# Kernel optimization log

Measured on AMD Instinct MI355X. Metric: run time of the kernel, lower is better.

The kernel has to match this reference:

```python
import jax, jax.numpy as jnp
import numpy as np

HIDDEN = 768
NUM_BLOCKS = 8
BLOCK = HIDDEN // NUM_BLOCKS
BASE_THR, K_DECAY, MIN_THR = 0.01, 20.0, 0.0005


def _threshold(height, width):
    # wavenumber-dependent soft-shrink threshold T(k), shape [H, W//2+1]
    fu = jnp.fft.fftfreq(height, d=1.0).astype(jnp.float32)[:, None]
    fv = jnp.fft.rfftfreq(width, d=1.0).astype(jnp.float32)[None, :]
    k = jnp.sqrt(fu ** 2 + fv ** 2) * max(height, width)
    thr = BASE_THR * jnp.exp(-0.5 * (k / K_DECAY) ** 2)
    return jnp.maximum(thr, MIN_THR)


def setup_inputs() -> dict:
    key = jax.random.key(0)
    kx, k1, k2, k3, k4 = jax.random.split(key, 5)
    scale = 0.02
    x = jax.random.normal(kx, (4, 128, 128, HIDDEN), dtype=jnp.float32)
    w1 = scale * jax.random.normal(k1, (2, NUM_BLOCKS, BLOCK, BLOCK), dtype=jnp.float32)
    b1 = scale * jax.random.normal(k2, (2, NUM_BLOCKS, BLOCK), dtype=jnp.float32)
    w2 = scale * jax.random.normal(k3, (2, NUM_BLOCKS, BLOCK, BLOCK), dtype=jnp.float32)
    b2 = scale * jax.random.normal(k4, (2, NUM_BLOCKS, BLOCK), dtype=jnp.float32)
    return {"x": x, "w1": w1, "b1": b1, "w2": w2, "b2": b2}


def reference(x, w1, b1, w2, b2):
    dtype = x.dtype
    bias = x
    xf = x.astype(jnp.float32)
    B, H, W, C = xf.shape
    Wc = W // 2 + 1
    # rfft2 over spatial dims, orthonormal
    Xc = jnp.fft.rfft2(xf, axes=(1, 2), norm='ortho')
    Xc = Xc.reshape(B, H, Wc, NUM_BLOCKS, BLOCK)
    xr, xi = jnp.real(Xc), jnp.imag(Xc)
    mm = lambda t, w: jnp.einsum('bhwni,nio->bhwno', t, w)
    # complex block-diagonal 2-layer MLP
    o1r = jax.nn.relu(mm(xr, w1[0]) - mm(xi, w1[1]) + b1[0])
    o1i = jax.nn.relu(mm(xi, w1[0]) + mm(xr, w1[1]) + b1[1])
    o2r = mm(o1r, w2[0]) - mm(o1i, w2[1]) + b2[0]
    o2i = mm(o1i, w2[0]) + mm(o1r, w2[1]) + b2[1]
    # soft-shrink on complex magnitude with wavenumber-dependent threshold
    mag = jnp.sqrt(o2r ** 2 + o2i ** 2 + 1e-8)
    thr = _threshold(H, W)[None, :, :, None, None]  # [1,H,Wc,1,1]
    sf = jax.nn.relu(mag - thr) / mag
    Yc = (o2r * sf) + 1j * (o2i * sf)
    Yc = Yc.reshape(B, H, Wc, C)
    y = jnp.fft.irfft2(Yc, s=(H, W), axes=(1, 2), norm='ortho')
    return y.astype(dtype) + bias
```

## Files before the change

kernel.cpp:

```cpp
#include <hip/hip_runtime.h>
#include <hip/hip_bf16.h>
#include <math.h>


#define HD   768
#define NBLK 8
#define HH   128
#define WW   128
#define WC   65
#define NPOS (HH * WC)

constexpr float SC    = 0.08838834764831845f;
constexpr float TWOPI = 6.28318530717958647692f;

constexpr int TM_OFF     = 0;
constexpr int TW_OFF     = 49152;
constexpr int TWI_OFF    = 69632;
constexpr int WF_OFF     = 90112;
constexpr int WF_END_U16 = 679936;
constexpr size_t A_UINTS = (size_t)4 * NPOS * HD;

typedef __attribute__((ext_vector_type(8))) short short8;
typedef __attribute__((ext_vector_type(4))) float f32x4;

#define MFMA __builtin_amdgcn_mfma_f32_16x16x32_bf16

static __device__ inline unsigned short f2bf(float f) {
  __hip_bfloat16 h = __float2bfloat16(f);
  return __builtin_bit_cast(unsigned short, h);
}
static __device__ inline unsigned int pack2(float re, float im) {
  return (unsigned int)f2bf(re) | ((unsigned int)f2bf(im) << 16);
}
static __device__ inline float lo2f(unsigned int u) {
  return __builtin_bit_cast(float, u << 16);
}
static __device__ inline float hi2f(unsigned int u) {
  return __builtin_bit_cast(float, u & 0xffff0000u);
}

__global__ __launch_bounds__(256) void k_prep(const float* __restrict__ w1,
                                              const float* __restrict__ b1,
                                              const float* __restrict__ w2,
                                              const float* __restrict__ b2,
                                              unsigned short* __restrict__ wf,
                                              float* __restrict__ bpk) {
  const int blk = blockIdx.x, t = threadIdx.x;
  if (blk < 16) {
    const int layer = blk >> 3, n = blk & 7;
    const float* w  = layer ? w2 : w1;
    const float* bs = layer ? b2 : b1;
    unsigned short* dst = wf + WF_OFF + (size_t)blk * (72 * 512);
    for (int e = t; e < 72 * 512; e += 256) {
      int f = e >> 9, idx = e & 511;
      int kk = f / 12, nt = f - kk * 12;
      int lane = idx >> 3, j = idx & 7;
      int k  = kk * 32 + (lane >> 4) * 8 + j;
      int cc = nt * 16 + (lane & 15);
      float v;
      if (k < 96) v = (cc < 96) ? w[(size_t)n * 9216 + k * 96 + cc]
                                : w[(size_t)(8 + n) * 9216 + k * 96 + (cc - 96)];
      else        v = (cc < 96) ? -w[(size_t)(8 + n) * 9216 + (k - 96) * 96 + cc]
                                :  w[(size_t)n * 9216 + (k - 96) * 96 + (cc - 96)];
      dst[e] = f2bf(v);
    }
    for (int c = t; c < 192; c += 256)
      bpk[blk * 192 + c] = (c < 96) ? bs[n * 96 + c] : bs[(8 + n) * 96 + (c - 96)];
  } else if (blk == 16) {
    for (int e = t; e < 96 * 512; e += 256) {
      int f = e >> 9, idx = e & 511;
      int part = f >> 5, rem = f & 31, kot = rem >> 2, kk = rem & 3;
      int lane = idx >> 3, j = idx & 7;
      int ko = kot * 16 + (lane & 15);
      int r  = kk * 32 + (lane >> 4) * 8 + j;
      float sn, cs; sincosf((TWOPI / 128.f) * (float)((ko * r) & 127), &sn, &cs);
      float v = (part == 0) ? cs : (part == 1) ? sn : -sn;
      wf[TM_OFF + (size_t)f * 512 + idx] = f2bf(v * SC);
    }
  } else if (blk == 17) {
    for (int e = t; e < 40 * 512; e += 256) {
      int f = e >> 9, idx = e & 511;
      int mt = f >> 2, kk = f & 3;
      int lane = idx >> 3, j = idx & 7;
      int row = mt * 16 + (lane & 15);
      int r   = kk * 32 + (lane >> 4) * 8 + j;
      int kor = (row < 80) ? row : row - 80;
      float sn, cs; sincosf((TWOPI / 128.f) * (float)((kor * r) & 127), &sn, &cs);
      wf[TW_OFF + (size_t)f * 512 + idx] = f2bf((row < 80 ? cs : -sn) * SC);
    }
  } else {
    for (int e = t; e < 40 * 512; e += 256) {
      int f = e >> 9, idx = e & 511;
      int mt = f / 5, kk = f - mt * 5;
      int lane = idx >> 3, j = idx & 7;
      int wr = mt * 16 + (lane & 15);
      int k  = kk * 32 + (lane >> 4) * 8 + j;
      float v = 0.f;
      if (k < 80) {
        int kb = k;
        if (kb <= 64) {
          float sn, cs; sincosf((TWOPI / 128.f) * (float)((wr * kb) & 127), &sn, &cs);
          v = SC * ((kb == 0 || kb == 64) ? 1.f : 2.f) * cs;
        }
      } else {
        int kb = k - 80;
        if (kb >= 1 && kb <= 63) {
          float sn, cs; sincosf((TWOPI / 128.f) * (float)((wr * kb) & 127), &sn, &cs);
          v = -2.f * SC * sn;
        }
      }
      wf[TWI_OFF + (size_t)f * 512 + idx] = f2bf(v);
    }
  }
}

__global__ __launch_bounds__(256) void k_fft_w(const float* __restrict__ x,
                                               unsigned int* __restrict__ A,
                                               const unsigned short* __restrict__ wf) {
  __shared__ unsigned short Xt[64 * 136];
  const int h = blockIdx.x, c0 = blockIdx.y * 64, b = blockIdx.z, t = threadIdx.x;
  const int wv = t >> 6, lane = t & 63, l15 = lane & 15, lg = lane >> 4;
  const float* xp = x + ((size_t)(b * HH + h)) * WW * HD + c0;
  for (int idx = t; idx < 128 * 64; idx += 256) {
    int r = idx >> 6, ch = idx & 63;
    Xt[ch * 136 + r] = f2bf(xp[(size_t)r * HD + ch]);
  }
  __syncthreads();
  const unsigned short* tw = wf + TW_OFF;
  f32x4 acc[10];
#pragma unroll
  for (int m = 0; m < 10; ++m) acc[m] = { 0.f, 0.f, 0.f, 0.f };
#pragma unroll
  for (int kk = 0; kk < 4; ++kk) {
    short8 bq = *(const short8*)&Xt[(wv * 16 + l15) * 136 + kk * 32 + lg * 8];
#pragma unroll
    for (int m = 0; m < 10; ++m) {
      short8 a = *(const short8*)&tw[(size_t)(m * 4 + kk) * 512 + lane * 8];
      acc[m] = MFMA(a, bq, acc[m], 0, 0, 0);
    }
  }
  unsigned int* Ao = A + ((size_t)b * NPOS + h * WC) * HD + c0 + wv * 16 + l15;
#pragma unroll
  for (int q = 0; q < 5; ++q)
#pragma unroll
    for (int r = 0; r < 4; ++r) {
      int ko = q * 16 + lg * 4 + r;
      if (ko <= 64) Ao[(size_t)ko * HD] = pack2(acc[q][r], acc[5 + q][r]);
    }
}

__global__ __launch_bounds__(256) void k_ifft_w(const unsigned int* __restrict__ A,
                                                const unsigned int* __restrict__ Bp,
                                                float* __restrict__ out,
                                                const unsigned short* __restrict__ wf) {
  __shared__ unsigned short Zt[64 * 168];
  const int h = blockIdx.x, c0 = blockIdx.y * 64, b = blockIdx.z, t = threadIdx.x;
  const int wv = t >> 6, lane = t & 63, l15 = lane & 15, lg = lane >> 4;
  const size_t base = ((size_t)b * NPOS + h * WC) * HD + c0;
  for (int idx = t; idx < 65 * 64; idx += 256) {
    int kb = idx >> 6, ch = idx & 63;
    unsigned int uA = A[base + (size_t)kb * HD + ch];
    unsigned int uB = Bp[base + (size_t)kb * HD + ch];
    float re = lo2f(uA) + lo2f(uB);
    float im = hi2f(uA) + hi2f(uB);
    Zt[ch * 168 + kb]      = f2bf(re);
    Zt[ch * 168 + 80 + kb] = (kb == 0 || kb == 64) ? (unsigned short)0 : f2bf(im);
  }
  for (int idx = t; idx < 64 * 32; idx += 256) {
    int ch = idx >> 5, q = idx & 31;
    if (q < 30) {
      int kb = 65 + (q % 15), half = q / 15;
      Zt[ch * 168 + half * 80 + kb] = 0;
    }
  }
  __syncthreads();
  const unsigned short* twi = wf + TWI_OFF;
  f32x4 acc[8];
#pragma unroll
  for (int m = 0; m < 8; ++m) acc[m] = { 0.f, 0.f, 0.f, 0.f };
#pragma unroll
  for (int kk = 0; kk < 5; ++kk) {
    short8 bq = *(const short8*)&Zt[(wv * 16 + l15) * 168 + kk * 32 + lg * 8];
#pragma unroll
    for (int m = 0; m < 8; ++m) {
      short8 a = *(const short8*)&twi[(size_t)(m * 5 + kk) * 512 + lane * 8];
      acc[m] = MFMA(a, bq, acc[m], 0, 0, 0);
    }
  }
#pragma unroll
  for (int m = 0; m < 8; ++m)
#pragma unroll
    for (int r = 0; r < 4; ++r) {
      int wr = m * 16 + lg * 4 + r;
      size_t go = (((size_t)(b * HH + h)) * WW + wr) * HD + c0 + wv * 16 + l15;
      out[go] = acc[m][r];
    }
}

template <int FWD>
static __device__ inline void dft_gemm8(const unsigned short* Rb, const unsigned short* Ib,
                                        const unsigned short* tm, int w, int lane,
                                        f32x4* aR, f32x4* aI) {
  const int l15 = lane & 15, lg = lane >> 4;
#pragma unroll
  for (int kkr = 0; kkr < 4; ++kkr) {
    const int r0 = kkr * 32 + lg * 8;
    short8 Ac = *(const short8*)&tm[(size_t)(0 * 32 + w * 4 + kkr) * 512 + lane * 8];
    short8 As = *(const short8*)&tm[(size_t)(1 * 32 + w * 4 + kkr) * 512 + lane * 8];
    short8 An = *(const short8*)&tm[(size_t)(2 * 32 + w * 4 + kkr) * 512 + lane * 8];
#pragma unroll
    for (int c = 0; c < 6; ++c) {
      short8 zr = *(const short8*)&Rb[(c * 16 + l15) * 136 + r0];
      short8 zi = *(const short8*)&Ib[(c * 16 + l15) * 136 + r0];
      aR[c] = MFMA(Ac, zr, aR[c], 0, 0, 0);
      if constexpr (FWD) {
        aR[c] = MFMA(As, zi, aR[c], 0, 0, 0);
        aI[c] = MFMA(Ac, zi, aI[c], 0, 0, 0);
        aI[c] = MFMA(An, zr, aI[c], 0, 0, 0);
      } else {
        aR[c] = MFMA(An, zi, aR[c], 0, 0, 0);
        aI[c] = MFMA(Ac, zi, aI[c], 0, 0, 0);
        aI[c] = MFMA(As, zr, aI[c], 0, 0, 0);
      }
    }
  }
}

__global__ __launch_bounds__(512) void k_mid(const unsigned int* __restrict__ A,
                                             unsigned int* __restrict__ Bp,
                                             const unsigned short* __restrict__ wf,
                                             const float* __restrict__ bpk) {
  __shared__ unsigned short Rb[13312], Ib[13312];
  __shared__ unsigned short WfX[2][12 * 512];
  const int kv = blockIdx.x, n = blockIdx.y, b = blockIdx.z, t = threadIdx.x;
  const int w = t >> 6, lane = t & 63, l15 = lane & 15, lg = lane >> 4;
  const size_t pbase = ((size_t)b * NPOS + kv) * HD + n * 96;
  const unsigned short* tm = wf + TM_OFF;
  const unsigned short* wf1 = wf + WF_OFF + (size_t)n * (72 * 512);
  const unsigned short* wf2 = wf + WF_OFF + (size_t)(8 + n) * (72 * 512);

#define LOAD_X(BUFI, SRC, KP)                                                    \
  for (int idx = t; idx < 768; idx += 512)                                       \
    ((int4*)WfX[BUFI])[idx] = ((const int4*)((SRC) + (KP) * 12 * 512))[idx];

  for (int idx = t; idx < 128 * 96; idx += 512) {
    int r = idx / 96, ch = idx - r * 96;
    unsigned int u = A[pbase + (size_t)r * (WC * HD) + ch];
    Rb[ch * 136 + r] = (unsigned short)(u & 0xffffu);
    Ib[ch * 136 + r] = (unsigned short)(u >> 16);
  }
  LOAD_X(0, wf1, 0);
  __syncthreads();

  f32x4 aR[6], aI[6];
#pragma unroll
  for (int c = 0; c < 6; ++c) { aR[c] = {0.f,0.f,0.f,0.f}; aI[c] = {0.f,0.f,0.f,0.f}; }
  dft_gemm8<1>(Rb, Ib, tm, w, lane, aR, aI);
  LOAD_X(1, wf1, 1);
  __syncthreads();

#pragma unroll
  for (int c = 0; c < 6; ++c)
#pragma unroll
    for (int r = 0; r < 4; ++r) {
      int row = w * 16 + lg * 4 + r, ch = c * 16 + l15;
      Rb[row * 104 + ch] = f2bf(aR[c][r]);
      Ib[row * 104 + ch] = f2bf(aI[c][r]);
    }

  const int row_a = (w * 16 + l15) * 104;
  f32x4 acc[12];
#pragma unroll
  for (int nt = 0; nt < 12; ++nt) {
    float bv = bpk[n * 192 + nt * 16 + l15];
    acc[nt] = { bv, bv, bv, bv };
  }

#define MLP_PAIR(BUF)                                                            \
  {                                                                              \
    short8 aRf = *(const short8*)&Rb[row_a + PK * 32 + lg * 8];                  \
    short8 aIf = *(const short8*)&Ib[row_a + PK * 32 + lg * 8];                  \
    _Pragma("unroll")                                                            \
    for (int nt = 0; nt < 12; ++nt) {                                            \
      short8 b0 = *(const short8*)&(BUF)[nt * 512 + lane * 8];                   \
      acc[nt] = MFMA(aRf, b0, acc[nt], 0, 0, 0);                                 \
      int nt2 = (nt < 6) ? nt + 6 : nt - 6;                                      \
      int4 nb = *(const int4*)&(BUF)[nt2 * 512 + lane * 8];                      \
      if (nt < 6) { nb.x ^= 0x80008000; nb.y ^= 0x80008000;                      \
                    nb.z ^= 0x80008000; nb.w ^= 0x80008000; }                    \
      acc[nt] = MFMA(aIf, __builtin_bit_cast(short8, nb), acc[nt], 0, 0, 0);     \
    }                                                                            \
  }

  { const int PK = 0; MLP_PAIR(WfX[0]); }
  { const int PK = 1; MLP_PAIR(WfX[1]); }
  __syncthreads();
  LOAD_X(0, wf1, 2);
  LOAD_X(1, wf2, 0);
  __syncthreads();
  { const int PK = 2; MLP_PAIR(WfX[0]); }

#pragma unroll
  for (int i = 0; i < 6; ++i)
#pragma unroll
    for (int r = 0; r < 4; ++r) {
      int row = w * 16 + lg * 4 + r, ch = i * 16 + l15;
      Rb[row * 104 + ch] = f2bf(fmaxf(acc[i][r], 0.f));
      Ib[row * 104 + ch] = f2bf(fmaxf(acc[6 + i][r], 0.f));
    }
#pragma unroll
  for (int nt = 0; nt < 12; ++nt) {
    float bv = bpk[(8 + n) * 192 + nt * 16 + l15];
    acc[nt] = { bv, bv, bv, bv };
  }
  __syncthreads();
  LOAD_X(0, wf2, 1);

  { const int PK = 0; MLP_PAIR(WfX[1]); }
  __syncthreads();
  LOAD_X(1, wf2, 2);
  { const int PK = 1; MLP_PAIR(WfX[0]); }
  __syncthreads();
  { const int PK = 2; MLP_PAIR(WfX[1]); }
  __syncthreads();

#pragma unroll
  for (int r = 0; r < 4; ++r) {
    int ko = w * 16 + lg * 4 + r;
    float kus = (ko >= 64) ? (float)(ko - 128) : (float)ko;
    float k2v = kus * kus + (float)(kv * kv);
    float thr = fmaxf(0.01f * expf(-0.00125f * k2v), 0.0005f);
#pragma unroll
    for (int i = 0; i < 6; ++i) {
      float mr = acc[i][r], mi = acc[6 + i][r];
      float mag = sqrtf(mr * mr + mi * mi + 1e-8f);
      float sf = fmaxf(mag - thr, 0.f) / mag;
      int ch = i * 16 + l15;
      Rb[ch * 136 + ko] = f2bf(mr * sf);
      Ib[ch * 136 + ko] = f2bf(mi * sf);
    }
  }
  __syncthreads();

#pragma unroll
  for (int c = 0; c < 6; ++c) { aR[c] = {0.f,0.f,0.f,0.f}; aI[c] = {0.f,0.f,0.f,0.f}; }
  dft_gemm8<0>(Rb, Ib, tm, w, lane, aR, aI);
#pragma unroll
  for (int c = 0; c < 6; ++c)
#pragma unroll
    for (int r = 0; r < 4; ++r) {
      int rr = w * 16 + lg * 4 + r, ch = c * 16 + l15;
      Bp[pbase + (size_t)rr * (WC * HD) + ch] = pack2(aR[c][r], aI[c][r]);
    }
#undef MLP_PAIR
#undef LOAD_X
}

extern "C" void kernel_launch(void* const* d_in, const int* in_sizes, int n_in,
                              void* d_out, int out_size, void* d_ws, size_t ws_size,
                              hipStream_t stream) {
  const float* x  = (const float*)d_in[0];
  const float* w1 = (const float*)d_in[1];
  const float* b1 = (const float*)d_in[2];
  const float* w2 = (const float*)d_in[3];
  const float* b2 = (const float*)d_in[4];
  float* out = (float*)d_out;
  unsigned int* A  = (unsigned int*)d_ws;
  unsigned int* Bp = A + A_UINTS;

  unsigned short* wf = (unsigned short*)(Bp + A_UINTS);
  float* bpk = (float*)(wf + WF_END_U16);

  k_prep<<<19, 256, 0, stream>>>(w1, b1, w2, b2, wf, bpk);
  k_fft_w<<<dim3(HH, HD / 64, 4), 256, 0, stream>>>(x, A, wf);
  k_mid<<<dim3(WC, NBLK, 4), 512, 0, stream>>>(A, Bp, wf, bpk);
  k_ifft_w<<<dim3(HH, HD / 64, 4), 256, 0, stream>>>(A, Bp, out, wf);
}
```

Measured before the change: 410.9 us.

## Single-buffer MLP weight tiles in LDS and XOR-swizzle spectral tiles

Replaces the double-buffered weight staging area with one buffer and adds barriers around each weight-chunk load, cutting LDS use per block by 12 KB, likely to fit more blocks per CU. It also applies an XOR swizzle to the channel-major spectral tiles used by the DFT GEMM to reduce LDS bank conflicts. The trade-off is that weight loads no longer overlap with MFMA work and the kernel has more syncthreads.

```diff
diff --git a/kernel.cpp b/kernel.cpp
--- a/kernel.cpp
+++ b/kernel.cpp
@@ -24,6 +24,8 @@
 typedef __attribute__((ext_vector_type(4))) float f32x4;
 
 #define MFMA __builtin_amdgcn_mfma_f32_16x16x32_bf16
+
+#define SWZ(ch, r) ((ch) * 136 + ((r) ^ (((ch) & 7) << 4)))
 
 static __device__ inline unsigned short f2bf(float f) {
   __hip_bfloat16 h = __float2bfloat16(f);
@@ -210,8 +212,9 @@
     short8 An = *(const short8*)&tm[(size_t)(2 * 32 + w * 4 + kkr) * 512 + lane * 8];
 #pragma unroll
     for (int c = 0; c < 6; ++c) {
-      short8 zr = *(const short8*)&Rb[(c * 16 + l15) * 136 + r0];
-      short8 zi = *(const short8*)&Ib[(c * 16 + l15) * 136 + r0];
+      const int ch = c * 16 + l15;
+      short8 zr = *(const short8*)&Rb[SWZ(ch, r0)];
+      short8 zi = *(const short8*)&Ib[SWZ(ch, r0)];
       aR[c] = MFMA(Ac, zr, aR[c], 0, 0, 0);
       if constexpr (FWD) {
         aR[c] = MFMA(As, zi, aR[c], 0, 0, 0);
@@ -231,7 +234,7 @@
                                              const unsigned short* __restrict__ wf,
                                              const float* __restrict__ bpk) {
   __shared__ unsigned short Rb[13312], Ib[13312];
-  __shared__ unsigned short WfX[2][12 * 512];
+  __shared__ unsigned short WfL[12 * 512];
   const int kv = blockIdx.x, n = blockIdx.y, b = blockIdx.z, t = threadIdx.x;
   const int w = t >> 6, lane = t & 63, l15 = lane & 15, lg = lane >> 4;
   const size_t pbase = ((size_t)b * NPOS + kv) * HD + n * 96;
@@ -239,24 +242,23 @@
   const unsigned short* wf1 = wf + WF_OFF + (size_t)n * (72 * 512);
   const unsigned short* wf2 = wf + WF_OFF + (size_t)(8 + n) * (72 * 512);
 
-#define LOAD_X(BUFI, SRC, KP)                                                    \
+#define LOAD_W(SRC, KP)                                                          \
   for (int idx = t; idx < 768; idx += 512)                                       \
-    ((int4*)WfX[BUFI])[idx] = ((const int4*)((SRC) + (KP) * 12 * 512))[idx];
+    ((int4*)WfL)[idx] = ((const int4*)((SRC) + (KP) * 12 * 512))[idx];
 
   for (int idx = t; idx < 128 * 96; idx += 512) {
     int r = idx / 96, ch = idx - r * 96;
     unsigned int u = A[pbase + (size_t)r * (WC * HD) + ch];
-    Rb[ch * 136 + r] = (unsigned short)(u & 0xffffu);
-    Ib[ch * 136 + r] = (unsigned short)(u >> 16);
-  }
-  LOAD_X(0, wf1, 0);
+    Rb[SWZ(ch, r)] = (unsigned short)(u & 0xffffu);
+    Ib[SWZ(ch, r)] = (unsigned short)(u >> 16);
+  }
+  LOAD_W(wf1, 0);
   __syncthreads();
 
   f32x4 aR[6], aI[6];
 #pragma unroll
   for (int c = 0; c < 6; ++c) { aR[c] = {0.f,0.f,0.f,0.f}; aI[c] = {0.f,0.f,0.f,0.f}; }
   dft_gemm8<1>(Rb, Ib, tm, w, lane, aR, aI);
-  LOAD_X(1, wf1, 1);
   __syncthreads();
 
 #pragma unroll
@@ -276,29 +278,31 @@
     acc[nt] = { bv, bv, bv, bv };
   }
 
-#define MLP_PAIR(BUF)                                                            \
+#define MLP_PAIR()                                                               \
   {                                                                              \
     short8 aRf = *(const short8*)&Rb[row_a + PK * 32 + lg * 8];                  \
     short8 aIf = *(const short8*)&Ib[row_a + PK * 32 + lg * 8];                  \
     _Pragma("unroll")                                                            \
     for (int nt = 0; nt < 12; ++nt) {                                            \
-      short8 b0 = *(const short8*)&(BUF)[nt * 512 + lane * 8];                   \
+      short8 b0 = *(const short8*)&WfL[nt * 512 + lane * 8];                     \
       acc[nt] = MFMA(aRf, b0, acc[nt], 0, 0, 0);                                 \
       int nt2 = (nt < 6) ? nt + 6 : nt - 6;                                      \
-      int4 nb = *(const int4*)&(BUF)[nt2 * 512 + lane * 8];                      \
+      int4 nb = *(const int4*)&WfL[nt2 * 512 + lane * 8];                        \
       if (nt < 6) { nb.x ^= 0x80008000; nb.y ^= 0x80008000;                      \
                     nb.z ^= 0x80008000; nb.w ^= 0x80008000; }                    \
       acc[nt] = MFMA(aIf, __builtin_bit_cast(short8, nb), acc[nt], 0, 0, 0);     \
     }                                                                            \
   }
 
-  { const int PK = 0; MLP_PAIR(WfX[0]); }
-  { const int PK = 1; MLP_PAIR(WfX[1]); }
-  __syncthreads();
-  LOAD_X(0, wf1, 2);
-  LOAD_X(1, wf2, 0);
-  __syncthreads();
-  { const int PK = 2; MLP_PAIR(WfX[0]); }
+  { const int PK = 0; MLP_PAIR(); }
+  __syncthreads();
+  LOAD_W(wf1, 1);
+  __syncthreads();
+  { const int PK = 1; MLP_PAIR(); }
+  __syncthreads();
+  LOAD_W(wf1, 2);
+  __syncthreads();
+  { const int PK = 2; MLP_PAIR(); }
 
 #pragma unroll
   for (int i = 0; i < 6; ++i)
@@ -314,14 +318,18 @@
     acc[nt] = { bv, bv, bv, bv };
   }
   __syncthreads();
-  LOAD_X(0, wf2, 1);
-
-  { const int PK = 0; MLP_PAIR(WfX[1]); }
-  __syncthreads();
-  LOAD_X(1, wf2, 2);
-  { const int PK = 1; MLP_PAIR(WfX[0]); }
-  __syncthreads();
-  { const int PK = 2; MLP_PAIR(WfX[1]); }
+  LOAD_W(wf2, 0);
+  __syncthreads();
+
+  { const int PK = 0; MLP_PAIR(); }
+  __syncthreads();
+  LOAD_W(wf2, 1);
+  __syncthreads();
+  { const int PK = 1; MLP_PAIR(); }
+  __syncthreads();
+  LOAD_W(wf2, 2);
+  __syncthreads();
+  { const int PK = 2; MLP_PAIR(); }
   __syncthreads();
 
 #pragma unroll
@@ -336,8 +344,8 @@
       float mag = sqrtf(mr * mr + mi * mi + 1e-8f);
       float sf = fmaxf(mag - thr, 0.f) / mag;
       int ch = i * 16 + l15;
-      Rb[ch * 136 + ko] = f2bf(mr * sf);
-      Ib[ch * 136 + ko] = f2bf(mi * sf);
+      Rb[SWZ(ch, ko)] = f2bf(mr * sf);
+      Ib[SWZ(ch, ko)] = f2bf(mi * sf);
     }
   }
   __syncthreads();
@@ -353,7 +361,7 @@
       Bp[pbase + (size_t)rr * (WC * HD) + ch] = pack2(aR[c][r], aI[c][r]);
     }
 #undef MLP_PAIR
-#undef LOAD_X
+#undef LOAD_W
 }
 
 extern "C" void kernel_launch(void* const* d_in, const int* in_sizes, int n_in,
```

Result: no change. 417.4 us (+1.6%).
